# Optimization experiments

Hardware: AMD Instinct MI355X
Metric: run time of the kernel (lower is better)

## Reference

```python
import jax, jax.numpy as jnp
import numpy as np

D_MODEL = 1024
N_HEADS = 16
D_HEAD = D_MODEL // N_HEADS


def setup_inputs() -> dict:
    key = jax.random.key(0)
    ks = jax.random.split(key, 12)
    B, S = 4, 2048
    n_fqk, n_fv = 2048, 1024
    n_rq, n_rk, n_val = 2048, 2048, 1024
    tk_qk, tk_v = 64, 32
    return {
        "x": jax.random.normal(ks[0], (B, S, D_MODEL), dtype=jnp.float32),
        "idx_qk": jax.random.randint(ks[1], (B, tk_qk), 0, n_fqk),
        "idx_v": jax.random.randint(ks[2], (B, tk_v), 0, n_fv),
        "idx_q": jax.random.randint(ks[3], (B, tk_qk), 0, n_rq),
        "idx_k": jax.random.randint(ks[4], (B, tk_qk), 0, n_rk),
        "idx_v2": jax.random.randint(ks[5], (B, tk_v), 0, n_val),
        "feature_qk_neurons": 0.02 * jax.random.normal(ks[6], (n_fqk, D_MODEL), dtype=jnp.float32),
        "feature_v_neurons": 0.02 * jax.random.normal(ks[7], (n_fv, D_MODEL), dtype=jnp.float32),
        "relational_q_neurons": 0.02 * jax.random.normal(ks[8], (n_rq, D_MODEL), dtype=jnp.float32),
        "relational_k_neurons": 0.02 * jax.random.normal(ks[9], (n_rk, D_MODEL), dtype=jnp.float32),
        "value_neurons": 0.02 * jax.random.normal(ks[10], (n_val, D_MODEL), dtype=jnp.float32),
        "W_O": 0.02 * jax.random.normal(ks[11], (D_MODEL, D_MODEL), dtype=jnp.float32),
    }


def reference(x, idx_qk, idx_v, idx_q, idx_k, idx_v2,
              feature_qk_neurons, feature_v_neurons,
              relational_q_neurons, relational_k_neurons,
              value_neurons, W_O):
    B, S, D = x.shape
    # Per-batch gathered compression projections: x [B,S,D] -> h [B,S,k]
    h_qk = jnp.einsum('bsd,bkd->bsk', x, feature_qk_neurons[idx_qk])
    h_v = jnp.einsum('bsd,bkd->bsk', x, feature_v_neurons[idx_v])
    # Expansion back to d_model
    Q = jnp.einsum('bsr,brd->bsd', h_qk, relational_q_neurons[idx_q])
    K = jnp.einsum('bsr,brd->bsd', h_qk, relational_k_neurons[idx_k])
    V = jnp.einsum('bsr,brd->bsd', h_v, value_neurons[idx_v2])
    # Multi-head split: [B,S,D] -> [B,H,S,dh]
    def split(t):
        return t.reshape(B, S, N_HEADS, D_HEAD).transpose(0, 2, 1, 3)
    Qh, Kh, Vh = split(Q), split(K), split(V)
    scale = 1.0 / jnp.sqrt(jnp.asarray(D_HEAD, dtype=x.dtype))
    scores = jnp.einsum('bhqd,bhkd->bhqk', Qh, Kh) * scale
    causal = jnp.tril(jnp.ones((S, S), dtype=bool))  # True = keep
    scores = jnp.where(causal, scores, jnp.finfo(scores.dtype).min)
    attn = jax.nn.softmax(scores, axis=-1)
    out = jnp.einsum('bhqk,bhkd->bhqd', attn, Vh)
    out = out.transpose(0, 2, 1, 3).reshape(B, S, D)
    return out @ W_O.T
```

## Files before the change

### kernel.cpp

```cpp
#include <hip/hip_runtime.h>
#include <hip/hip_bf16.h>

typedef __hip_bfloat16 bf16;
typedef __attribute__((ext_vector_type(8))) short bf16x8;
typedef __attribute__((ext_vector_type(4))) float f32x4;

#define NB 4
#define NS 2048
#define ND 1024
#define NH 16
#define DH 64
#define KQK 64
#define KV 32

#define QSCALE 0.18033688011112042f

__device__ __forceinline__ unsigned int pk2(float a, float b) {
  unsigned short ua = __bfloat16_as_ushort(__float2bfloat16(a));
  unsigned short ub = __bfloat16_as_ushort(__float2bfloat16(b));
  return (unsigned int)ua | ((unsigned int)ub << 16);
}
__device__ __forceinline__ bf16x8 cvt8(float4 a, float4 b) {
  union { unsigned int u[4]; bf16x8 v; } r;
  r.u[0] = pk2(a.x, a.y); r.u[1] = pk2(a.z, a.w);
  r.u[2] = pk2(b.x, b.y); r.u[3] = pk2(b.z, b.w);
  return r.v;
}

__global__ __launch_bounds__(256) void h_direct(
    const float* __restrict__ x,
    const int* __restrict__ idx_qk, const int* __restrict__ idx_v,
    const float* __restrict__ Fqk, const float* __restrict__ Fv,
    bf16* __restrict__ h_qk, bf16* __restrict__ h_v) {
  const int s0 = (blockIdx.x & 127) * 16;
  const int b  = blockIdx.x >> 7;
  const int tid = threadIdx.x, w = tid >> 6, l = tid & 63;
  const int lr = l & 15, lg = l >> 4;

  __shared__ float Red[4][16][100];

  const float* wrow[6];
#pragma unroll
  for (int nt = 0; nt < 6; ++nt) {
    int n = nt * 16 + lr;
    int idx = (n < KQK) ? idx_qk[b * KQK + n] : idx_v[b * KV + n - KQK];
    wrow[nt] = ((n < KQK) ? Fqk : Fv) + (size_t)idx * ND;
  }
  const float* xrow = x + ((size_t)b * NS + s0 + lr) * ND;

  f32x4 acc[6];
#pragma unroll
  for (int nt = 0; nt < 6; ++nt) acc[nt] = (f32x4)(0.f);

  const int kbase = w * 256;
  for (int kc = 0; kc < 8; ++kc) {
    const int k0 = kbase + kc * 32 + lg * 8;
    float4 xa = *(const float4*)(xrow + k0);
    float4 xb = *(const float4*)(xrow + k0 + 4);
    bf16x8 af = cvt8(xa, xb);
#pragma unroll
    for (int nt = 0; nt < 6; ++nt) {
      float4 wa = *(const float4*)(wrow[nt] + k0);
      float4 wb = *(const float4*)(wrow[nt] + k0 + 4);
      acc[nt] = __builtin_amdgcn_mfma_f32_16x16x32_bf16(af, cvt8(wa, wb), acc[nt], 0, 0, 0);
    }
  }

#pragma unroll
  for (int nt = 0; nt < 6; ++nt)
#pragma unroll
    for (int r = 0; r < 4; ++r)
      Red[w][lg * 4 + r][nt * 16 + lr] = acc[nt][r];
  __syncthreads();

  const int s = tid >> 4, nb0 = tid & 15;
#pragma unroll
  for (int j = 0; j < 6; ++j) {
    int n = nb0 + 16 * j;
    float v = Red[0][s][n] + Red[1][s][n] + Red[2][s][n] + Red[3][s][n];
    size_t row = (size_t)b * NS + s0 + s;
    if (n < KQK) h_qk[row * KQK + n] = __float2bfloat16(v);
    else         h_v[row * KV + n - KQK] = __float2bfloat16(v);
  }
}

__global__ __launch_bounds__(256) void wcvt(const float* __restrict__ W,
                                            bf16* __restrict__ Wb) {
  int i = blockIdx.x * 256 + threadIdx.x;
  float4 t = reinterpret_cast<const float4*>(W)[i];
  reinterpret_cast<uint2*>(Wb)[i] = make_uint2(pk2(t.x, t.y), pk2(t.z, t.w));
}

__global__ __launch_bounds__(256) void expand_mfma(
    const bf16* __restrict__ hqk, const bf16* __restrict__ hv,
    const float* __restrict__ RQ, const float* __restrict__ RK,
    const float* __restrict__ VN,
    const int* __restrict__ idx_q, const int* __restrict__ idx_k,
    const int* __restrict__ idx_v2,
    bf16* __restrict__ Qb, bf16* __restrict__ Kb, bf16* __restrict__ Vb) {
  const int s0 = blockIdx.x * 128, d0 = blockIdx.y * 128, b = blockIdx.z;
  const int tid = threadIdx.x, w = tid >> 6, l = tid & 63;
  const int lr = l & 15, lg = l >> 4;
  const int wm = w >> 1, wn = w & 1;

  __shared__ __align__(16) short Ah[128][72];
  __shared__ __align__(16) short Av[128][40];
  __shared__ __align__(16) short Wt[128][72];

  for (int i = tid; i < 1024; i += 256) {
    int r = i >> 3, c = i & 7;
    *(bf16x8*)&Ah[r][c * 8] = *(const bf16x8*)((const short*)hqk + ((size_t)b * NS + s0 + r) * KQK + c * 8);
  }
  for (int i = tid; i < 512; i += 256) {
    int r = i >> 2, c = i & 3;
    *(bf16x8*)&Av[r][c * 8] = *(const bf16x8*)((const short*)hv + ((size_t)b * NS + s0 + r) * KV + c * 8);
  }

  auto stageW = [&](const float* Wsrc, const int* idxv, int KR) {
    for (int i = tid; i < KR * 16; i += 256) {
      int r = i & (KR - 1), dc = i / KR;
      const float* src = Wsrc + (size_t)idxv[b * KR + r] * ND + d0 + dc * 8;
      float4 t0 = *(const float4*)src;
      float4 t1 = *(const float4*)(src + 4);
      Wt[dc * 8 + 0][r] = __bfloat16_as_ushort(__float2bfloat16(t0.x));
      Wt[dc * 8 + 1][r] = __bfloat16_as_ushort(__float2bfloat16(t0.y));
      Wt[dc * 8 + 2][r] = __bfloat16_as_ushort(__float2bfloat16(t0.z));
      Wt[dc * 8 + 3][r] = __bfloat16_as_ushort(__float2bfloat16(t0.w));
      Wt[dc * 8 + 4][r] = __bfloat16_as_ushort(__float2bfloat16(t1.x));
      Wt[dc * 8 + 5][r] = __bfloat16_as_ushort(__float2bfloat16(t1.y));
      Wt[dc * 8 + 6][r] = __bfloat16_as_ushort(__float2bfloat16(t1.z));
      Wt[dc * 8 + 7][r] = __bfloat16_as_ushort(__float2bfloat16(t1.w));
    }
  };

  auto computeQK = [&](float scale, bf16* outp) {
    f32x4 acc[4][4];
#pragma unroll
    for (int mt = 0; mt < 4; ++mt)
#pragma unroll
      for (int nt = 0; nt < 4; ++nt) acc[mt][nt] = (f32x4)(0.f);
#pragma unroll
    for (int c2 = 0; c2 < 2; ++c2) {
      bf16x8 af[4], bfv[4];
#pragma unroll
      for (int t = 0; t < 4; ++t) {
        af[t]  = *(const bf16x8*)&Ah[wm * 64 + t * 16 + lr][c2 * 32 + lg * 8];
        bfv[t] = *(const bf16x8*)&Wt[wn * 64 + t * 16 + lr][c2 * 32 + lg * 8];
      }
#pragma unroll
      for (int mt = 0; mt < 4; ++mt)
#pragma unroll
        for (int nt = 0; nt < 4; ++nt)
          acc[mt][nt] = __builtin_amdgcn_mfma_f32_16x16x32_bf16(af[mt], bfv[nt], acc[mt][nt], 0, 0, 0);
    }
#pragma unroll
    for (int mt = 0; mt < 4; ++mt)
#pragma unroll
      for (int rr = 0; rr < 4; ++rr) {
        size_t row = (size_t)b * NS + s0 + wm * 64 + mt * 16 + lg * 4 + rr;
        short* orow = (short*)outp + row * ND + d0 + wn * 64;
#pragma unroll
        for (int nt = 0; nt < 4; ++nt)
          orow[nt * 16 + lr] = __bfloat16_as_ushort(__float2bfloat16(acc[mt][nt][rr] * scale));
      }
  };

  stageW(RQ, idx_q, 64);
  __syncthreads();
  computeQK(QSCALE, Qb);
  __syncthreads();
  stageW(RK, idx_k, 64);
  __syncthreads();
  computeQK(1.0f, Kb);
  __syncthreads();
  stageW(VN, idx_v2, 32);
  __syncthreads();
  {
    f32x4 acc[4][4];
#pragma unroll
    for (int mt = 0; mt < 4; ++mt)
#pragma unroll
      for (int nt = 0; nt < 4; ++nt) acc[mt][nt] = (f32x4)(0.f);
    bf16x8 af[4], bfv[4];
#pragma unroll
    for (int t = 0; t < 4; ++t) {
      af[t]  = *(const bf16x8*)&Av[wm * 64 + t * 16 + lr][lg * 8];
      bfv[t] = *(const bf16x8*)&Wt[wn * 64 + t * 16 + lr][lg * 8];
    }
#pragma unroll
    for (int mt = 0; mt < 4; ++mt)
#pragma unroll
      for (int nt = 0; nt < 4; ++nt)
        acc[mt][nt] = __builtin_amdgcn_mfma_f32_16x16x32_bf16(af[mt], bfv[nt], acc[mt][nt], 0, 0, 0);
#pragma unroll
    for (int mt = 0; mt < 4; ++mt)
#pragma unroll
      for (int rr = 0; rr < 4; ++rr) {
        size_t row = (size_t)b * NS + s0 + wm * 64 + mt * 16 + lg * 4 + rr;
        short* orow = (short*)Vb + row * ND + d0 + wn * 64;
#pragma unroll
        for (int nt = 0; nt < 4; ++nt)
          orow[nt * 16 + lr] = __bfloat16_as_ushort(__float2bfloat16(acc[mt][nt][rr]));
      }
  }
}

__global__ __launch_bounds__(512, 4) void attn_mfma(
    const bf16* __restrict__ Q, const bf16* __restrict__ K,
    const bf16* __restrict__ V, bf16* __restrict__ out) {
  const int wg = blockIdx.x;
  const int swz = (wg & 7) * 64 + (wg >> 3);
  const int pr = swz & 7, hh = (swz >> 3) & 15, b = swz >> 7;
  const int tid = threadIdx.x, wq = tid >> 6, l = tid & 63;
  const int lr = l & 15, lg = l >> 4;

  __shared__ __align__(16) short Ks[2][64][72];
  __shared__ __align__(16) short Vt[2][64][72];
  __shared__ __align__(16) short Ps[8][16][72];

  const short* Qp = (const short*)Q + (size_t)(b * NS) * ND + hh * DH;
  const short* Kp = (const short*)K + (size_t)(b * NS) * ND + hh * DH;
  const short* Vp = (const short*)V + (size_t)(b * NS) * ND + hh * DH;

  const int krow = tid >> 3, kcol = (tid & 7) * 8;
  const int vk = tid & 63, vd = (tid >> 6) * 8;
  bf16x8 kreg, vreg;

  auto LOAD = [&](int kt) {
    kreg = *(const bf16x8*)(Kp + (size_t)(kt * 64 + krow) * ND + kcol);
    vreg = *(const bf16x8*)(Vp + (size_t)(kt * 64 + vk) * ND + vd);
  };
  auto WRITE = [&](int buf) {
    *(bf16x8*)&Ks[buf][krow][kcol] = kreg;
#pragma unroll
    for (int j = 0; j < 8; ++j) Vt[buf][vd + j][vk] = vreg[j];
  };

  for (int pass = 0; pass < 2; ++pass) {
    const int qt = pass ? (15 - pr) : pr;
    const int q0 = qt * 128;

    bf16x8 qf[2];
    {
      const short* qrow = Qp + (size_t)(q0 + wq * 16 + lr) * ND;
      qf[0] = *(const bf16x8*)(qrow + lg * 8);
      qf[1] = *(const bf16x8*)(qrow + 32 + lg * 8);
    }
    f32x4 Oacc[4];
#pragma unroll
    for (int dt = 0; dt < 4; ++dt) Oacc[dt] = (f32x4)(0.f);
    float l_r = 0.f;

    const int NT = 2 * qt + 2;
    const int wlast = 2 * qt + (wq >> 2);

    LOAD(0);
    WRITE(0);
    __syncthreads();

    for (int kt = 0; kt < NT; ++kt) {
      const int cur = kt & 1;
      const bool more = (kt + 1 < NT);
      if (more) LOAD(kt + 1);

      if (kt <= wlast) {
        f32x4 s[4];
#pragma unroll
        for (int t = 0; t < 4; ++t) {
          bf16x8 kf0 = *(const bf16x8*)&Ks[cur][t * 16 + lr][lg * 8];
          bf16x8 kf1 = *(const bf16x8*)&Ks[cur][t * 16 + lr][32 + lg * 8];
          f32x4 a = __builtin_amdgcn_mfma_f32_16x16x32_bf16(kf0, qf[0], (f32x4)(0.f), 0, 0, 0);
          s[t] = __builtin_amdgcn_mfma_f32_16x16x32_bf16(kf1, qf[1], a, 0, 0, 0);
        }
        const bool diag = (kt == wlast);
        float p[4][4];
        if (diag) {
          const int qg = q0 + wq * 16 + lr;
#pragma unroll
          for (int t = 0; t < 4; ++t)
#pragma unroll
            for (int r = 0; r < 4; ++r) {
              float sv = s[t][r];
              if ((kt * 64 + t * 16 + lg * 4 + r) > qg) sv = -1e30f;
              float pv = exp2f(fminf(sv, 88.f));
              p[t][r] = pv;
              l_r += pv;
            }
        } else {
#pragma unroll
          for (int t = 0; t < 4; ++t)
#pragma unroll
            for (int r = 0; r < 4; ++r) {
              float pv = exp2f(fminf(s[t][r], 88.f));
              p[t][r] = pv;
              l_r += pv;
            }
        }
#pragma unroll
        for (int t = 0; t < 4; ++t)
          *(uint2*)&Ps[wq][lr][t * 16 + lg * 4] =
              make_uint2(pk2(p[t][0], p[t][1]), pk2(p[t][2], p[t][3]));
        bf16x8 pa0 = *(const bf16x8*)&Ps[wq][lr][lg * 8];
        bf16x8 pa1 = *(const bf16x8*)&Ps[wq][lr][32 + lg * 8];
#pragma unroll
        for (int dt = 0; dt < 4; ++dt) {
          bf16x8 vf0 = *(const bf16x8*)&Vt[cur][dt * 16 + lr][lg * 8];
          bf16x8 vf1 = *(const bf16x8*)&Vt[cur][dt * 16 + lr][32 + lg * 8];
          Oacc[dt] = __builtin_amdgcn_mfma_f32_16x16x32_bf16(pa0, vf0, Oacc[dt], 0, 0, 0);
          Oacc[dt] = __builtin_amdgcn_mfma_f32_16x16x32_bf16(pa1, vf1, Oacc[dt], 0, 0, 0);
        }
      }
      if (more) WRITE((kt + 1) & 1);
      __syncthreads();
    }

    float lf = l_r;
    lf += __shfl_xor(lf, 16, 64);
    lf += __shfl_xor(lf, 32, 64);
    const float linv = 1.f / fmaxf(lf, 1e-35f);
#pragma unroll
    for (int r = 0; r < 4; ++r) {
      float lb = __shfl(linv, (l & 48) | (lg * 4 + r), 64);
      size_t row = (size_t)(b * NS) + q0 + wq * 16 + lg * 4 + r;
      short* orow = (short*)out + row * ND + hh * DH;
#pragma unroll
      for (int dt = 0; dt < 4; ++dt)
        orow[dt * 16 + lr] = __bfloat16_as_ushort(__float2bfloat16(Oacc[dt][r] * lb));
    }
  }
}

__global__ __launch_bounds__(256) void out_gemm_mfma(
    const bf16* __restrict__ A, const bf16* __restrict__ W,
    float* __restrict__ C) {
  const int m0 = blockIdx.x * 128, i0 = blockIdx.y * 128;
  const int tid = threadIdx.x, w = tid >> 6, l = tid & 63;
  const int lr = l & 15, lg = l >> 4;
  const int wm = w >> 1, wn = w & 1;

  __shared__ __align__(16) short As[128][72];
  __shared__ __align__(16) short Bs[128][72];

  f32x4 acc[4][4];
#pragma unroll
  for (int a = 0; a < 4; ++a)
#pragma unroll
    for (int bb = 0; bb < 4; ++bb) acc[a][bb] = (f32x4)(0.f);

  for (int j0 = 0; j0 < ND; j0 += 64) {
    __syncthreads();
    for (int v = tid; v < 1024; v += 256) {
      int r = v >> 3, c = v & 7;
      *(bf16x8*)&As[r][c * 8] = *(const bf16x8*)((const short*)A + ((size_t)m0 + r) * ND + j0 + c * 8);
      *(bf16x8*)&Bs[r][c * 8] = *(const bf16x8*)((const short*)W + ((size_t)i0 + r) * ND + j0 + c * 8);
    }
    __syncthreads();
#pragma unroll
    for (int c2 = 0; c2 < 2; ++c2) {
      bf16x8 af[4], bfv[4];
#pragma unroll
      for (int t = 0; t < 4; ++t) {
        af[t]  = *(const bf16x8*)&As[wm * 64 + t * 16 + lr][c2 * 32 + lg * 8];
        bfv[t] = *(const bf16x8*)&Bs[wn * 64 + t * 16 + lr][c2 * 32 + lg * 8];
      }
#pragma unroll
      for (int mt = 0; mt < 4; ++mt)
#pragma unroll
        for (int nt = 0; nt < 4; ++nt)
          acc[mt][nt] = __builtin_amdgcn_mfma_f32_16x16x32_bf16(af[mt], bfv[nt], acc[mt][nt], 0, 0, 0);
    }
  }
#pragma unroll
  for (int mt = 0; mt < 4; ++mt)
#pragma unroll
    for (int r = 0; r < 4; ++r) {
      size_t row = (size_t)m0 + wm * 64 + mt * 16 + lg * 4 + r;
#pragma unroll
      for (int nt = 0; nt < 4; ++nt)
        C[row * ND + i0 + wn * 64 + nt * 16 + lr] = acc[mt][nt][r];
    }
}

extern "C" void kernel_launch(void* const* d_in, const int* in_sizes, int n_in,
                              void* d_out, int out_size, void* d_ws, size_t ws_size,
                              hipStream_t stream) {
  const float* x      = (const float*)d_in[0];
  const int* idx_qk   = (const int*)d_in[1];
  const int* idx_v    = (const int*)d_in[2];
  const int* idx_q    = (const int*)d_in[3];
  const int* idx_k    = (const int*)d_in[4];
  const int* idx_v2   = (const int*)d_in[5];
  const float* Fqk    = (const float*)d_in[6];
  const float* Fv     = (const float*)d_in[7];
  const float* RQ     = (const float*)d_in[8];
  const float* RK     = (const float*)d_in[9];
  const float* VN     = (const float*)d_in[10];
  const float* W_O    = (const float*)d_in[11];

  bf16* h_qk = (bf16*)d_ws;
  bf16* h_v  = h_qk + (size_t)NB * NS * KQK;
  bf16* Qb   = h_v + (size_t)NB * NS * KV;
  bf16* Kb   = Qb + (size_t)NB * NS * ND;
  bf16* Vb   = Kb + (size_t)NB * NS * ND;
  bf16* Ob   = Vb + (size_t)NB * NS * ND;
  bf16* Wb   = Ob + (size_t)NB * NS * ND;

  h_direct<<<dim3(NB * NS / 16), 256, 0, stream>>>(x, idx_qk, idx_v, Fqk, Fv, h_qk, h_v);
  wcvt<<<ND * ND / 4 / 256, 256, 0, stream>>>(W_O, Wb);

  expand_mfma<<<dim3(NS / 128, ND / 128, NB), 256, 0, stream>>>(
      h_qk, h_v, RQ, RK, VN, idx_q, idx_k, idx_v2, Qb, Kb, Vb);

  attn_mfma<<<dim3(8 * NH * NB), 512, 0, stream>>>(Qb, Kb, Vb, Ob);

  out_gemm_mfma<<<dim3(NB * NS / 128, ND / 128), 256, 0, stream>>>(Ob, Wb, (float*)d_out);
}
```

Before: 158.2 us.

## Stage x and gathered feature rows in shared memory for compression GEMM

The compression projection kernel now converts tiles of x and the gathered feature rows to bf16 in LDS, then runs MFMA on them. This replaces the design where every wave read weights straight from global memory with a split-K cross-wave reduction. Each block covers 32 sequence rows instead of 16, and the four waves split the M×N tile, so each block loads the weight rows once and the reduction step goes away. In exchange there are two barriers per K-step, a serial K loop of 16 steps, and half as many blocks.

```diff
diff --git a/kernel.cpp b/kernel.cpp
--- a/kernel.cpp
+++ b/kernel.cpp
@@ -20,67 +20,68 @@
   unsigned short ub = __bfloat16_as_ushort(__float2bfloat16(b));
   return (unsigned int)ua | ((unsigned int)ub << 16);
 }
-__device__ __forceinline__ bf16x8 cvt8(float4 a, float4 b) {
-  union { unsigned int u[4]; bf16x8 v; } r;
-  r.u[0] = pk2(a.x, a.y); r.u[1] = pk2(a.z, a.w);
-  r.u[2] = pk2(b.x, b.y); r.u[3] = pk2(b.z, b.w);
-  return r.v;
-}
-
-__global__ __launch_bounds__(256) void h_direct(
+
+__global__ __launch_bounds__(256) void h_staged(
     const float* __restrict__ x,
     const int* __restrict__ idx_qk, const int* __restrict__ idx_v,
     const float* __restrict__ Fqk, const float* __restrict__ Fv,
     bf16* __restrict__ h_qk, bf16* __restrict__ h_v) {
-  const int s0 = (blockIdx.x & 127) * 16;
-  const int b  = blockIdx.x >> 7;
+  const int s0 = (blockIdx.x & 63) * 32;
+  const int b  = blockIdx.x >> 6;
   const int tid = threadIdx.x, w = tid >> 6, l = tid & 63;
   const int lr = l & 15, lg = l >> 4;
 
-  __shared__ float Red[4][16][100];
-
-  const float* wrow[6];
-#pragma unroll
-  for (int nt = 0; nt < 6; ++nt) {
-    int n = nt * 16 + lr;
-    int idx = (n < KQK) ? idx_qk[b * KQK + n] : idx_v[b * KV + n - KQK];
-    wrow[nt] = ((n < KQK) ? Fqk : Fv) + (size_t)idx * ND;
-  }
-  const float* xrow = x + ((size_t)b * NS + s0 + lr) * ND;
-
-  f32x4 acc[6];
-#pragma unroll
-  for (int nt = 0; nt < 6; ++nt) acc[nt] = (f32x4)(0.f);
-
-  const int kbase = w * 256;
-  for (int kc = 0; kc < 8; ++kc) {
-    const int k0 = kbase + kc * 32 + lg * 8;
-    float4 xa = *(const float4*)(xrow + k0);
-    float4 xb = *(const float4*)(xrow + k0 + 4);
-    bf16x8 af = cvt8(xa, xb);
-#pragma unroll
-    for (int nt = 0; nt < 6; ++nt) {
-      float4 wa = *(const float4*)(wrow[nt] + k0);
-      float4 wb = *(const float4*)(wrow[nt] + k0 + 4);
-      acc[nt] = __builtin_amdgcn_mfma_f32_16x16x32_bf16(af, cvt8(wa, wb), acc[nt], 0, 0, 0);
-    }
-  }
-
-#pragma unroll
-  for (int nt = 0; nt < 6; ++nt)
-#pragma unroll
-    for (int r = 0; r < 4; ++r)
-      Red[w][lg * 4 + r][nt * 16 + lr] = acc[nt][r];
-  __syncthreads();
-
-  const int s = tid >> 4, nb0 = tid & 15;
-#pragma unroll
-  for (int j = 0; j < 6; ++j) {
-    int n = nb0 + 16 * j;
-    float v = Red[0][s][n] + Red[1][s][n] + Red[2][s][n] + Red[3][s][n];
-    size_t row = (size_t)b * NS + s0 + s;
-    if (n < KQK) h_qk[row * KQK + n] = __float2bfloat16(v);
-    else         h_v[row * KV + n - KQK] = __float2bfloat16(v);
+  __shared__ __align__(16) short Xs[32][72];
+  __shared__ __align__(16) short Ws[96][72];
+  __shared__ const float* rowp[96];
+
+  if (tid < 96) {
+    rowp[tid] = (tid < 64) ? Fqk + (size_t)idx_qk[b * KQK + tid] * ND
+                           : Fv  + (size_t)idx_v [b * KV + tid - 64] * ND;
+  }
+
+  const int wm = w >> 1, wn0 = (w & 1) * 3;
+  f32x4 acc[3];
+#pragma unroll
+  for (int nt = 0; nt < 3; ++nt) acc[nt] = (f32x4)(0.f);
+
+  const int xr = tid >> 3, xc = (tid & 7) * 8;
+  for (int k0 = 0; k0 < ND; k0 += 64) {
+    __syncthreads();
+    {
+      const float* src = x + ((size_t)b * NS + s0 + xr) * ND + k0 + xc;
+      float4 a0 = *(const float4*)src, a1 = *(const float4*)(src + 4);
+      *(uint2*)&Xs[xr][xc]     = make_uint2(pk2(a0.x, a0.y), pk2(a0.z, a0.w));
+      *(uint2*)&Xs[xr][xc + 4] = make_uint2(pk2(a1.x, a1.y), pk2(a1.z, a1.w));
+    }
+    for (int v = tid; v < 768; v += 256) {
+      int r = v >> 3, c = (v & 7) * 8;
+      const float* src = rowp[r] + k0 + c;
+      float4 a0 = *(const float4*)src, a1 = *(const float4*)(src + 4);
+      *(uint2*)&Ws[r][c]     = make_uint2(pk2(a0.x, a0.y), pk2(a0.z, a0.w));
+      *(uint2*)&Ws[r][c + 4] = make_uint2(pk2(a1.x, a1.y), pk2(a1.z, a1.w));
+    }
+    __syncthreads();
+#pragma unroll
+    for (int c2 = 0; c2 < 2; ++c2) {
+      bf16x8 af = *(const bf16x8*)&Xs[wm * 16 + lr][c2 * 32 + lg * 8];
+#pragma unroll
+      for (int nt = 0; nt < 3; ++nt) {
+        bf16x8 bfv = *(const bf16x8*)&Ws[(wn0 + nt) * 16 + lr][c2 * 32 + lg * 8];
+        acc[nt] = __builtin_amdgcn_mfma_f32_16x16x32_bf16(af, bfv, acc[nt], 0, 0, 0);
+      }
+    }
+  }
+
+#pragma unroll
+  for (int r = 0; r < 4; ++r) {
+    const size_t row = (size_t)b * NS + s0 + wm * 16 + lg * 4 + r;
+#pragma unroll
+    for (int nt = 0; nt < 3; ++nt) {
+      int n = (wn0 + nt) * 16 + lr;
+      if (n < KQK) h_qk[row * KQK + n] = __float2bfloat16(acc[nt][r]);
+      else         h_v[row * KV + n - KQK] = __float2bfloat16(acc[nt][r]);
+    }
   }
 }
 
@@ -405,7 +406,7 @@
   bf16* Ob   = Vb + (size_t)NB * NS * ND;
   bf16* Wb   = Ob + (size_t)NB * NS * ND;
 
-  h_direct<<<dim3(NB * NS / 16), 256, 0, stream>>>(x, idx_qk, idx_v, Fqk, Fv, h_qk, h_v);
+  h_staged<<<dim3(NB * NS / 32), 256, 0, stream>>>(x, idx_qk, idx_v, Fqk, Fv, h_qk, h_v);
   wcvt<<<ND * ND / 4 / 256, 256, 0, stream>>>(W_O, Wb);
 
   expand_mfma<<<dim3(NS / 128, ND / 128, NB), 256, 0, stream>>>(
```

Result: slower. 164.1 us (+3.7%).
